# Kernel optimization log

Measured on AMD Instinct MI355X. Metric: run time of the kernel, lower is better.

Reference implementation:

```python
import jax, jax.numpy as jnp
import numpy as np

IN_DIM, H_DIM = 512, 1024
SEQ, BS = 512, 128

def setup_inputs() -> dict:
    key = jax.random.key(0)
    ks = jax.random.split(key, 8)
    d = IN_DIM + H_DIM
    s = 1.0 / np.sqrt(d)
    return {
        "x": jax.random.normal(ks[0], (SEQ, BS, IN_DIM), jnp.float32),
        "h0": jax.random.normal(ks[1], (BS, H_DIM), jnp.float32),
        # Linear weights stored as [in_features, out_features] for x @ W
        "Wz": jax.random.uniform(ks[2], (d, H_DIM), jnp.float32, -s, s),
        "bz": jax.random.uniform(ks[3], (H_DIM,), jnp.float32, -s, s),
        "Wr": jax.random.uniform(ks[4], (d, H_DIM), jnp.float32, -s, s),
        "br": jax.random.uniform(ks[5], (H_DIM,), jnp.float32, -s, s),
        "Wh": jax.random.uniform(ks[6], (d, H_DIM), jnp.float32, -s, s),
        "bh": jax.random.uniform(ks[7], (H_DIM,), jnp.float32, -s, s),
    }

def reference(x, h0, Wz, bz, Wr, br, Wh, bh):
    # Non-standard GRU cell: softmax-activated update/reset gates.
    def step(h, xt):
        hx = jnp.concatenate([h, xt], axis=1)          # [bs, h+in]
        z = jax.nn.softmax(hx @ Wz + bz, axis=1)       # [bs, h]
        r = jax.nn.softmax(hx @ Wr + br, axis=1)
        rhx = jnp.concatenate([r * h, xt], axis=1)
        h_new = (1.0 - z) * h + z * jnp.tanh(rhx @ Wh + bh)
        return h_new, h_new
    _, out = jax.lax.scan(step, h0, x)                 # out: [seq, bs, h]
    return out
```

## Files before the change

### kernel.cpp

```cpp
#include <hip/hip_runtime.h>
#include <hip/hip_bf16.h>


#define SEQ 512
#define BS 128
#define IN_DIM 512
#define H_DIM 1024
#define DTOT 1536
#define NZR 2048

typedef __attribute__((ext_vector_type(8))) short bfrag;
typedef __attribute__((ext_vector_type(4))) float facc;

__device__ __forceinline__ unsigned short f2bf(float f) {
    unsigned int u = __float_as_uint(f);
    unsigned int r = (u + 0x7FFFu + ((u >> 16) & 1u)) >> 16;
    return (unsigned short)r;
}


__global__ void cvt_w(const float* __restrict__ Wz, const float* __restrict__ Wr,
                      const float* __restrict__ Wh,
                      unsigned short* __restrict__ wzr, unsigned short* __restrict__ wh) {
    size_t i = (size_t)blockIdx.x * 256 + threadIdx.x;
    if (i >= (size_t)3072 * DTOT) return;
    int k = (int)(i % DTOT);
    int n = (int)(i / DTOT);
    float v;
    if (n < 1024)       v = Wz[(size_t)k * H_DIM + n];
    else if (n < 2048)  v = Wr[(size_t)k * H_DIM + (n - 1024)];
    else                v = Wh[(size_t)k * H_DIM + (n - 2048)];
    unsigned short b = f2bf(v);
    if (n < 2048) wzr[(size_t)n * DTOT + k] = b;
    else          wh[(size_t)(n - 2048) * DTOT + k] = b;
}

__global__ void cvt_x(const float4* __restrict__ x, unsigned long long* __restrict__ xb) {
    size_t i = (size_t)blockIdx.x * 256 + threadIdx.x;
    if (i >= (size_t)SEQ * BS * IN_DIM / 4) return;
    float4 v = x[i];
    unsigned long long p = (unsigned long long)f2bf(v.x)
                         | ((unsigned long long)f2bf(v.y) << 16)
                         | ((unsigned long long)f2bf(v.z) << 32)
                         | ((unsigned long long)f2bf(v.w) << 48);
    xb[i] = p;
}

__global__ void init_h(const float* __restrict__ h0, float* __restrict__ hf,
                       unsigned short* __restrict__ hb) {
    int i = blockIdx.x * 256 + threadIdx.x;
    if (i >= BS * H_DIM) return;
    float v = h0[i];
    hf[i] = v;
    hb[i] = f2bf(v);
}


__global__ __launch_bounds__(256) void gemm_zr(
    const unsigned short* __restrict__ hb,
    const unsigned short* __restrict__ xb,
    const unsigned short* __restrict__ wt,
    const float* __restrict__ bz, const float* __restrict__ br,
    float* __restrict__ pre) {
    const int lane = threadIdx.x & 63;
    const int wid  = threadIdx.x >> 6;
    const int nBase = blockIdx.x * 64 + wid * 16;
    const int mBase = blockIdx.y * 64;
    const int lm = lane & 15;
    const int kq = lane >> 4;
    facc acc[4];
    #pragma unroll
    for (int i = 0; i < 4; ++i) acc[i] = (facc){0.f, 0.f, 0.f, 0.f};
    const unsigned short* wrow = wt + (size_t)(nBase + lm) * DTOT + kq * 8;
    #pragma unroll 4
    for (int kc = 0; kc < DTOT; kc += 32) {
        const unsigned short* asrc;
        int astride;
        if (kc < 1024) { asrc = hb + kc;          astride = H_DIM; }
        else           { asrc = xb + (kc - 1024); astride = IN_DIM; }
        bfrag b = *(const bfrag*)(wrow + kc);
        #pragma unroll
        for (int mt = 0; mt < 4; ++mt) {
            bfrag a = *(const bfrag*)(asrc + (size_t)(mBase + mt * 16 + lm) * astride + kq * 8);
            acc[mt] = __builtin_amdgcn_mfma_f32_16x16x32_bf16(a, b, acc[mt], 0, 0, 0);
        }
    }
    const int col = nBase + lm;
    const float bias = (col < 1024) ? bz[col] : br[col - 1024];
    #pragma unroll
    for (int mt = 0; mt < 4; ++mt) {
        #pragma unroll
        for (int r = 0; r < 4; ++r) {
            int row = mBase + mt * 16 + kq * 4 + r;
            pre[(size_t)row * NZR + col] = acc[mt][r] + bias;
        }
    }
}

__global__ __launch_bounds__(256) void softmax_rh(
    const float* __restrict__ pre, const float* __restrict__ hf,
    float* __restrict__ z, unsigned short* __restrict__ rh) {
    const int b = blockIdx.x;
    const int tid = threadIdx.x;
    const int lane = tid & 63, wid = tid >> 6;
    const float* prow = pre + (size_t)b * NZR;
    float zl[4], rl[4];
    float mz = -1e30f, mr = -1e30f;
    #pragma unroll
    for (int j = 0; j < 4; ++j) {
        int n = tid + j * 256;
        zl[j] = prow[n];
        rl[j] = prow[1024 + n];
        mz = fmaxf(mz, zl[j]); mr = fmaxf(mr, rl[j]);
    }
    #pragma unroll
    for (int off = 32; off; off >>= 1) {
        mz = fmaxf(mz, __shfl_down(mz, off, 64));
        mr = fmaxf(mr, __shfl_down(mr, off, 64));
    }
    __shared__ float sm[8];
    if (lane == 0) { sm[wid] = mz; sm[4 + wid] = mr; }
    __syncthreads();
    mz = fmaxf(fmaxf(sm[0], sm[1]), fmaxf(sm[2], sm[3]));
    mr = fmaxf(fmaxf(sm[4], sm[5]), fmaxf(sm[6], sm[7]));
    float sz = 0.f, sr = 0.f;
    #pragma unroll
    for (int j = 0; j < 4; ++j) {
        zl[j] = expf(zl[j] - mz); rl[j] = expf(rl[j] - mr);
        sz += zl[j]; sr += rl[j];
    }
    #pragma unroll
    for (int off = 32; off; off >>= 1) {
        sz += __shfl_down(sz, off, 64);
        sr += __shfl_down(sr, off, 64);
    }
    __shared__ float ss[8];
    if (lane == 0) { ss[wid] = sz; ss[4 + wid] = sr; }
    __syncthreads();
    sz = ss[0] + ss[1] + ss[2] + ss[3];
    sr = ss[4] + ss[5] + ss[6] + ss[7];
    const float inz = 1.0f / sz, inr = 1.0f / sr;
    #pragma unroll
    for (int j = 0; j < 4; ++j) {
        int n = tid + j * 256;
        size_t idx = (size_t)b * H_DIM + n;
        z[idx] = zl[j] * inz;
        rh[idx] = f2bf(rl[j] * inr * hf[idx]);
    }
}

__global__ __launch_bounds__(256) void gemm_h(
    const unsigned short* __restrict__ rh,
    const unsigned short* __restrict__ xb,
    const unsigned short* __restrict__ wt,
    const float* __restrict__ bh,
    const float* __restrict__ z,
    float* __restrict__ hf, unsigned short* __restrict__ hb,
    float* __restrict__ out) {
    const int lane = threadIdx.x & 63;
    const int wid  = threadIdx.x >> 6;
    const int nBase = blockIdx.x * 64 + wid * 16;
    const int mBase = blockIdx.y * 64;
    const int lm = lane & 15;
    const int kq = lane >> 4;
    facc acc[4];
    #pragma unroll
    for (int i = 0; i < 4; ++i) acc[i] = (facc){0.f, 0.f, 0.f, 0.f};
    const unsigned short* wrow = wt + (size_t)(nBase + lm) * DTOT + kq * 8;
    #pragma unroll 4
    for (int kc = 0; kc < DTOT; kc += 32) {
        const unsigned short* asrc;
        int astride;
        if (kc < 1024) { asrc = rh + kc;          astride = H_DIM; }
        else           { asrc = xb + (kc - 1024); astride = IN_DIM; }
        bfrag b = *(const bfrag*)(wrow + kc);
        #pragma unroll
        for (int mt = 0; mt < 4; ++mt) {
            bfrag a = *(const bfrag*)(asrc + (size_t)(mBase + mt * 16 + lm) * astride + kq * 8);
            acc[mt] = __builtin_amdgcn_mfma_f32_16x16x32_bf16(a, b, acc[mt], 0, 0, 0);
        }
    }
    const int col = nBase + lm;
    const float bias = bh[col];
    #pragma unroll
    for (int mt = 0; mt < 4; ++mt) {
        #pragma unroll
        for (int r = 0; r < 4; ++r) {
            int row = mBase + mt * 16 + kq * 4 + r;
            size_t idx = (size_t)row * H_DIM + col;
            float th = tanhf(acc[mt][r] + bias);
            float zv = z[idx];
            float hv = hf[idx];
            float hn = fmaf(zv, th - hv, hv);
            hf[idx] = hn;
            hb[idx] = f2bf(hn);
            out[idx] = hn;
        }
    }
}


extern "C" void kernel_launch(void* const* d_in, const int* in_sizes, int n_in,
                              void* d_out, int out_size, void* d_ws, size_t ws_size,
                              hipStream_t stream) {
    const float* x  = (const float*)d_in[0];
    const float* h0 = (const float*)d_in[1];
    const float* Wz = (const float*)d_in[2];
    const float* bz = (const float*)d_in[3];
    const float* Wr = (const float*)d_in[4];
    const float* br = (const float*)d_in[5];
    const float* Wh = (const float*)d_in[6];
    const float* bh = (const float*)d_in[7];
    float* out = (float*)d_out;

    char* base = (char*)d_ws;
    unsigned short* wzr_t  = (unsigned short*)(base);
    unsigned short* wh_t   = (unsigned short*)(base + 6291456);
    unsigned short* x_bf16 = (unsigned short*)(base + 9437184);
    float*          h_f32  = (float*)         (base + 76546048);
    unsigned short* h_bf16 = (unsigned short*)(base + 77070336);
    unsigned short* rh_b   = (unsigned short*)(base + 77332480);
    float*          pre_zr = (float*)         (base + 77594624);
    float*          z_f32  = (float*)         (base + 78643200);

    cvt_w<<<(3072 * DTOT + 255) / 256, 256, 0, stream>>>(Wz, Wr, Wh, wzr_t, wh_t);
    cvt_x<<<((SEQ * BS * IN_DIM / 4) + 255) / 256, 256, 0, stream>>>(
        (const float4*)x, (unsigned long long*)x_bf16);
    init_h<<<(BS * H_DIM + 255) / 256, 256, 0, stream>>>(h0, h_f32, h_bf16);

    for (int t = 0; t < SEQ; ++t) {
        const unsigned short* xb_t = x_bf16 + (size_t)t * BS * IN_DIM;
        float* out_t = out + (size_t)t * BS * H_DIM;
        gemm_zr<<<dim3(NZR / 64, BS / 64), 256, 0, stream>>>(
            h_bf16, xb_t, wzr_t, bz, br, pre_zr);
        softmax_rh<<<BS, 256, 0, stream>>>(pre_zr, h_f32, z_f32, rh_b);
        gemm_h<<<dim3(H_DIM / 64, BS / 64), 256, 0, stream>>>(
            rh_b, xb_t, wh_t, bh, z_f32, h_f32, h_bf16, out_t);
    }
}
```

Baseline: 34.89 ms.

## Replace per-step kernel launches with persistent cooperative GRU kernel using grid barriers

Replaces the three-kernels-per-timestep loop with one cooperative persistent kernel of 192 blocks. Each block keeps its 16-column weight slice resident in LDS and synchronises timesteps with a software grid barrier. Softmax is computed without max subtraction, using partial row sums reduced across blocks, and the x-projection for the next step is overlapped with the h-gate work. This removes about 1500 launches and the weight reloads from global memory, at the risk of exp overflow without a max and of barrier latency dominating each step.

```diff
diff --git a/kernel.cpp b/kernel.cpp
--- a/kernel.cpp
+++ b/kernel.cpp
@@ -1,5 +1,4 @@
 #include <hip/hip_runtime.h>
-#include <hip/hip_bf16.h>
 
 
 #define SEQ 512
@@ -7,7 +6,9 @@
 #define IN_DIM 512
 #define H_DIM 1024
 #define DTOT 1536
-#define NZR 2048
+#define NB 192
+#define NT 512
+#define WPAD 1544
 
 typedef __attribute__((ext_vector_type(8))) short bfrag;
 typedef __attribute__((ext_vector_type(4))) float facc;
@@ -47,8 +48,9 @@
 }
 
 __global__ void init_h(const float* __restrict__ h0, float* __restrict__ hf,
-                       unsigned short* __restrict__ hb) {
+                       unsigned short* __restrict__ hb, unsigned* __restrict__ bar) {
     int i = blockIdx.x * 256 + threadIdx.x;
+    if (i < 2) bar[i] = 0u;
     if (i >= BS * H_DIM) return;
     float v = h0[i];
     hf[i] = v;
@@ -56,146 +58,214 @@
 }
 
 
-__global__ __launch_bounds__(256) void gemm_zr(
-    const unsigned short* __restrict__ hb,
-    const unsigned short* __restrict__ xb,
-    const unsigned short* __restrict__ wt,
-    const float* __restrict__ bz, const float* __restrict__ br,
-    float* __restrict__ pre) {
-    const int lane = threadIdx.x & 63;
-    const int wid  = threadIdx.x >> 6;
-    const int nBase = blockIdx.x * 64 + wid * 16;
-    const int mBase = blockIdx.y * 64;
-    const int lm = lane & 15;
-    const int kq = lane >> 4;
-    facc acc[4];
-    #pragma unroll
-    for (int i = 0; i < 4; ++i) acc[i] = (facc){0.f, 0.f, 0.f, 0.f};
-    const unsigned short* wrow = wt + (size_t)(nBase + lm) * DTOT + kq * 8;
-    #pragma unroll 4
-    for (int kc = 0; kc < DTOT; kc += 32) {
-        const unsigned short* asrc;
-        int astride;
-        if (kc < 1024) { asrc = hb + kc;          astride = H_DIM; }
-        else           { asrc = xb + (kc - 1024); astride = IN_DIM; }
-        bfrag b = *(const bfrag*)(wrow + kc);
+struct PArgs {
+    const unsigned short* wzr;
+    const unsigned short* wh;
+    const unsigned short* xb;
+    const float* bz;
+    const float* br;
+    const float* bh;
+    float* hf;
+    unsigned short* hb;
+    unsigned short* ub;
+    float* ez;
+    float* szp;
+    float* srp;
+    float* out;
+    unsigned* bar;
+};
+
+__device__ __forceinline__ void gridbar(unsigned* cnt, unsigned* gen) {
+    __builtin_amdgcn_fence(__ATOMIC_RELEASE, "agent");
+    __syncthreads();
+    if (threadIdx.x == 0) {
+        unsigned g = __hip_atomic_load(gen, __ATOMIC_RELAXED, __HIP_MEMORY_SCOPE_AGENT);
+        unsigned a = __hip_atomic_fetch_add(cnt, 1u, __ATOMIC_ACQ_REL, __HIP_MEMORY_SCOPE_AGENT);
+        if (a == (unsigned)(NB - 1)) {
+            __hip_atomic_store(cnt, 0u, __ATOMIC_RELAXED, __HIP_MEMORY_SCOPE_AGENT);
+            __hip_atomic_store(gen, g + 1u, __ATOMIC_RELEASE, __HIP_MEMORY_SCOPE_AGENT);
+        } else {
+            while (__hip_atomic_load(gen, __ATOMIC_RELAXED, __HIP_MEMORY_SCOPE_AGENT) == g) {
+                __builtin_amdgcn_s_sleep(2);
+            }
+        }
+    }
+    __syncthreads();
+    __builtin_amdgcn_fence(__ATOMIC_ACQUIRE, "agent");
+}
+
+__global__ __launch_bounds__(NT, 1) void gru_persistent(PArgs p) {
+    __shared__ unsigned short wlds[16][WPAD];
+    __shared__ float redz[4][BS];
+    __shared__ float redr[4][BS];
+    __shared__ float invz[BS];
+    __shared__ float invr[BS];
+
+    const int tid  = threadIdx.x;
+    const int lane = tid & 63;
+    const int wv   = tid >> 6;
+    const int lm   = lane & 15;
+    const int kq   = lane >> 4;
+    const int blk  = blockIdx.x;
+    const bool is_h = (blk >= 128);
+    const bool is_z = (blk < 64);
+    const int arow = wv * 16 + lm;
+
+    const unsigned short* wsrc = is_h ? (p.wh + (size_t)(blk - 128) * 16 * DTOT)
+                                      : (p.wzr + (size_t)blk * 16 * DTOT);
+    for (int c = tid; c < 16 * 192; c += NT) {
+        int n = c / 192;
+        int o = (c % 192) * 8;
+        *(float4*)&wlds[n][o] = *(const float4*)(wsrc + (size_t)n * DTOT + o);
+    }
+    float bias_l;
+    if (is_h) {
+        bias_l = p.bh[(blk - 128) * 16 + lm];
+    } else {
+        int n = blk * 16 + lm;
+        bias_l = (n < H_DIM) ? p.bz[n] : p.br[n - H_DIM];
+    }
+    __syncthreads();
+
+    unsigned* cnt = p.bar;
+    unsigned* gen = p.bar + 1;
+
+    facc accx = (facc){0.f, 0.f, 0.f, 0.f};
+    if (!is_h) {
+        const unsigned short* ax = p.xb + (size_t)arow * IN_DIM + kq * 8;
         #pragma unroll
-        for (int mt = 0; mt < 4; ++mt) {
-            bfrag a = *(const bfrag*)(asrc + (size_t)(mBase + mt * 16 + lm) * astride + kq * 8);
-            acc[mt] = __builtin_amdgcn_mfma_f32_16x16x32_bf16(a, b, acc[mt], 0, 0, 0);
+        for (int kc = 0; kc < IN_DIM; kc += 32) {
+            bfrag a = *(const bfrag*)(ax + kc);
+            bfrag b = *(const bfrag*)&wlds[lm][H_DIM + kc + kq * 8];
+            accx = __builtin_amdgcn_mfma_f32_16x16x32_bf16(a, b, accx, 0, 0, 0);
         }
     }
-    const int col = nBase + lm;
-    const float bias = (col < 1024) ? bz[col] : br[col - 1024];
-    #pragma unroll
-    for (int mt = 0; mt < 4; ++mt) {
-        #pragma unroll
-        for (int r = 0; r < 4; ++r) {
-            int row = mBase + mt * 16 + kq * 4 + r;
-            pre[(size_t)row * NZR + col] = acc[mt][r] + bias;
+
+    for (int t = 0; t < SEQ; ++t) {
+        const unsigned short* xb_t = p.xb + (size_t)t * BS * IN_DIM;
+
+        if (!is_h) {
+            facc accA = accx;
+            facc accB = (facc){0.f, 0.f, 0.f, 0.f};
+            const unsigned short* ah = p.hb + (size_t)arow * H_DIM + kq * 8;
+            #pragma unroll 4
+            for (int kc = 0; kc < H_DIM; kc += 64) {
+                bfrag a0 = *(const bfrag*)(ah + kc);
+                bfrag b0 = *(const bfrag*)&wlds[lm][kc + kq * 8];
+                accA = __builtin_amdgcn_mfma_f32_16x16x32_bf16(a0, b0, accA, 0, 0, 0);
+                bfrag a1 = *(const bfrag*)(ah + kc + 32);
+                bfrag b1 = *(const bfrag*)&wlds[lm][kc + 32 + kq * 8];
+                accB = __builtin_amdgcn_mfma_f32_16x16x32_bf16(a1, b1, accB, 0, 0, 0);
+            }
+            accA = accA + accB;
+            float e[4], sf[4];
+            #pragma unroll
+            for (int r = 0; r < 4; ++r) {
+                e[r] = expf(accA[r] + bias_l);
+                float s = e[r];
+                s += __shfl_xor(s, 1, 64);
+                s += __shfl_xor(s, 2, 64);
+                s += __shfl_xor(s, 4, 64);
+                s += __shfl_xor(s, 8, 64);
+                sf[r] = s;
+            }
+            if (is_z) {
+                const int col = blk * 16 + lm;
+                #pragma unroll
+                for (int r = 0; r < 4; ++r) {
+                    const int rr = wv * 16 + kq * 4 + r;
+                    p.ez[(size_t)rr * H_DIM + col] = e[r];
+                }
+                if (lm == 0) {
+                    #pragma unroll
+                    for (int r = 0; r < 4; ++r)
+                        p.szp[(size_t)blk * BS + wv * 16 + kq * 4 + r] = sf[r];
+                }
+            } else {
+                const int col = (blk - 64) * 16 + lm;
+                #pragma unroll
+                for (int r = 0; r < 4; ++r) {
+                    const int rr = wv * 16 + kq * 4 + r;
+                    float u = e[r] * p.hf[(size_t)rr * H_DIM + col];
+                    p.ub[(size_t)rr * H_DIM + col] = f2bf(u);
+                }
+                if (lm == 0) {
+                    #pragma unroll
+                    for (int r = 0; r < 4; ++r)
+                        p.srp[(size_t)(blk - 64) * BS + wv * 16 + kq * 4 + r] = sf[r];
+                }
+            }
+        } else {
+            accx = (facc){0.f, 0.f, 0.f, 0.f};
+            const unsigned short* ax = xb_t + (size_t)arow * IN_DIM + kq * 8;
+            #pragma unroll
+            for (int kc = 0; kc < IN_DIM; kc += 32) {
+                bfrag a = *(const bfrag*)(ax + kc);
+                bfrag b = *(const bfrag*)&wlds[lm][H_DIM + kc + kq * 8];
+                accx = __builtin_amdgcn_mfma_f32_16x16x32_bf16(a, b, accx, 0, 0, 0);
+            }
         }
-    }
-}
-
-__global__ __launch_bounds__(256) void softmax_rh(
-    const float* __restrict__ pre, const float* __restrict__ hf,
-    float* __restrict__ z, unsigned short* __restrict__ rh) {
-    const int b = blockIdx.x;
-    const int tid = threadIdx.x;
-    const int lane = tid & 63, wid = tid >> 6;
-    const float* prow = pre + (size_t)b * NZR;
-    float zl[4], rl[4];
-    float mz = -1e30f, mr = -1e30f;
-    #pragma unroll
-    for (int j = 0; j < 4; ++j) {
-        int n = tid + j * 256;
-        zl[j] = prow[n];
-        rl[j] = prow[1024 + n];
-        mz = fmaxf(mz, zl[j]); mr = fmaxf(mr, rl[j]);
-    }
-    #pragma unroll
-    for (int off = 32; off; off >>= 1) {
-        mz = fmaxf(mz, __shfl_down(mz, off, 64));
-        mr = fmaxf(mr, __shfl_down(mr, off, 64));
-    }
-    __shared__ float sm[8];
-    if (lane == 0) { sm[wid] = mz; sm[4 + wid] = mr; }
-    __syncthreads();
-    mz = fmaxf(fmaxf(sm[0], sm[1]), fmaxf(sm[2], sm[3]));
-    mr = fmaxf(fmaxf(sm[4], sm[5]), fmaxf(sm[6], sm[7]));
-    float sz = 0.f, sr = 0.f;
-    #pragma unroll
-    for (int j = 0; j < 4; ++j) {
-        zl[j] = expf(zl[j] - mz); rl[j] = expf(rl[j] - mr);
-        sz += zl[j]; sr += rl[j];
-    }
-    #pragma unroll
-    for (int off = 32; off; off >>= 1) {
-        sz += __shfl_down(sz, off, 64);
-        sr += __shfl_down(sr, off, 64);
-    }
-    __shared__ float ss[8];
-    if (lane == 0) { ss[wid] = sz; ss[4 + wid] = sr; }
-    __syncthreads();
-    sz = ss[0] + ss[1] + ss[2] + ss[3];
-    sr = ss[4] + ss[5] + ss[6] + ss[7];
-    const float inz = 1.0f / sz, inr = 1.0f / sr;
-    #pragma unroll
-    for (int j = 0; j < 4; ++j) {
-        int n = tid + j * 256;
-        size_t idx = (size_t)b * H_DIM + n;
-        z[idx] = zl[j] * inz;
-        rh[idx] = f2bf(rl[j] * inr * hf[idx]);
-    }
-}
-
-__global__ __launch_bounds__(256) void gemm_h(
-    const unsigned short* __restrict__ rh,
-    const unsigned short* __restrict__ xb,
-    const unsigned short* __restrict__ wt,
-    const float* __restrict__ bh,
-    const float* __restrict__ z,
-    float* __restrict__ hf, unsigned short* __restrict__ hb,
-    float* __restrict__ out) {
-    const int lane = threadIdx.x & 63;
-    const int wid  = threadIdx.x >> 6;
-    const int nBase = blockIdx.x * 64 + wid * 16;
-    const int mBase = blockIdx.y * 64;
-    const int lm = lane & 15;
-    const int kq = lane >> 4;
-    facc acc[4];
-    #pragma unroll
-    for (int i = 0; i < 4; ++i) acc[i] = (facc){0.f, 0.f, 0.f, 0.f};
-    const unsigned short* wrow = wt + (size_t)(nBase + lm) * DTOT + kq * 8;
-    #pragma unroll 4
-    for (int kc = 0; kc < DTOT; kc += 32) {
-        const unsigned short* asrc;
-        int astride;
-        if (kc < 1024) { asrc = rh + kc;          astride = H_DIM; }
-        else           { asrc = xb + (kc - 1024); astride = IN_DIM; }
-        bfrag b = *(const bfrag*)(wrow + kc);
-        #pragma unroll
-        for (int mt = 0; mt < 4; ++mt) {
-            bfrag a = *(const bfrag*)(asrc + (size_t)(mBase + mt * 16 + lm) * astride + kq * 8);
-            acc[mt] = __builtin_amdgcn_mfma_f32_16x16x32_bf16(a, b, acc[mt], 0, 0, 0);
+        gridbar(cnt, gen);
+
+        if (is_h) {
+            {
+                const int b = tid & 127;
+                const int g = tid >> 7;
+                float az = 0.f, ar = 0.f;
+                #pragma unroll
+                for (int j = 0; j < 16; ++j) {
+                    az += p.szp[(size_t)(g * 16 + j) * BS + b];
+                    ar += p.srp[(size_t)(g * 16 + j) * BS + b];
+                }
+                redz[g][b] = az;
+                redr[g][b] = ar;
+            }
+            __syncthreads();
+            if (tid < BS) {
+                invz[tid] = 1.f / (redz[0][tid] + redz[1][tid] + redz[2][tid] + redz[3][tid]);
+                invr[tid] = 1.f / (redr[0][tid] + redr[1][tid] + redr[2][tid] + redr[3][tid]);
+            }
+            __syncthreads();
+            facc accA = (facc){0.f, 0.f, 0.f, 0.f};
+            facc accB = (facc){0.f, 0.f, 0.f, 0.f};
+            const unsigned short* au = p.ub + (size_t)arow * H_DIM + kq * 8;
+            #pragma unroll 4
+            for (int kc = 0; kc < H_DIM; kc += 64) {
+                bfrag a0 = *(const bfrag*)(au + kc);
+                bfrag b0 = *(const bfrag*)&wlds[lm][kc + kq * 8];
+                accA = __builtin_amdgcn_mfma_f32_16x16x32_bf16(a0, b0, accA, 0, 0, 0);
+                bfrag a1 = *(const bfrag*)(au + kc + 32);
+                bfrag b1 = *(const bfrag*)&wlds[lm][kc + 32 + kq * 8];
+                accB = __builtin_amdgcn_mfma_f32_16x16x32_bf16(a1, b1, accB, 0, 0, 0);
+            }
+            accA = accA + accB;
+            const int col = (blk - 128) * 16 + lm;
+            float* out_t = p.out + (size_t)t * BS * H_DIM;
+            #pragma unroll
+            for (int r = 0; r < 4; ++r) {
+                const int rr = wv * 16 + kq * 4 + r;
+                const size_t idx = (size_t)rr * H_DIM + col;
+                float pre = accA[r] * invr[rr] + accx[r] + bias_l;
+                float th = tanhf(pre);
+                float zv = p.ez[idx] * invz[rr];
+                float hv = p.hf[idx];
+                float hn = fmaf(zv, th - hv, hv);
+                p.hf[idx] = hn;
+                p.hb[idx] = f2bf(hn);
+                out_t[idx] = hn;
+            }
+        } else if (t + 1 < SEQ) {
+            accx = (facc){0.f, 0.f, 0.f, 0.f};
+            const unsigned short* ax = p.xb + (size_t)(t + 1) * BS * IN_DIM
+                                       + (size_t)arow * IN_DIM + kq * 8;
+            #pragma unroll
+            for (int kc = 0; kc < IN_DIM; kc += 32) {
+                bfrag a = *(const bfrag*)(ax + kc);
+                bfrag b = *(const bfrag*)&wlds[lm][H_DIM + kc + kq * 8];
+                accx = __builtin_amdgcn_mfma_f32_16x16x32_bf16(a, b, accx, 0, 0, 0);
+            }
         }
-    }
-    const int col = nBase + lm;
-    const float bias = bh[col];
-    #pragma unroll
-    for (int mt = 0; mt < 4; ++mt) {
-        #pragma unroll
-        for (int r = 0; r < 4; ++r) {
-            int row = mBase + mt * 16 + kq * 4 + r;
-            size_t idx = (size_t)row * H_DIM + col;
-            float th = tanhf(acc[mt][r] + bias);
-            float zv = z[idx];
-            float hv = hf[idx];
-            float hn = fmaf(zv, th - hv, hv);
-            hf[idx] = hn;
-            hb[idx] = f2bf(hn);
-            out[idx] = hn;
-        }
+        gridbar(cnt, gen);
     }
 }
 
@@ -214,27 +284,28 @@
     float* out = (float*)d_out;
 
     char* base = (char*)d_ws;
-    unsigned short* wzr_t  = (unsigned short*)(base);
-    unsigned short* wh_t   = (unsigned short*)(base + 6291456);
-    unsigned short* x_bf16 = (unsigned short*)(base + 9437184);
-    float*          h_f32  = (float*)         (base + 76546048);
-    unsigned short* h_bf16 = (unsigned short*)(base + 77070336);
-    unsigned short* rh_b   = (unsigned short*)(base + 77332480);
-    float*          pre_zr = (float*)         (base + 77594624);
-    float*          z_f32  = (float*)         (base + 78643200);
+    unsigned short* wzr_t = (unsigned short*)(base);
+    unsigned short* wh_t  = (unsigned short*)(base + 6291456);
+    unsigned short* x_b   = (unsigned short*)(base + 9437184);
+    float*          h_f32 = (float*)         (base + 76546048);
+    unsigned short* h_b   = (unsigned short*)(base + 77070336);
+    unsigned short* u_b   = (unsigned short*)(base + 77332480);
+    float*          ez    = (float*)         (base + 77594624);
+    float*          szp   = (float*)         (base + 78118912);
+    float*          srp   = (float*)         (base + 78151680);
+    unsigned*       bar   = (unsigned*)      (base + 78184448);
 
     cvt_w<<<(3072 * DTOT + 255) / 256, 256, 0, stream>>>(Wz, Wr, Wh, wzr_t, wh_t);
     cvt_x<<<((SEQ * BS * IN_DIM / 4) + 255) / 256, 256, 0, stream>>>(
-        (const float4*)x, (unsigned long long*)x_bf16);
-    init_h<<<(BS * H_DIM + 255) / 256, 256, 0, stream>>>(h0, h_f32, h_bf16);
-
-    for (int t = 0; t < SEQ; ++t) {
-        const unsigned short* xb_t = x_bf16 + (size_t)t * BS * IN_DIM;
-        float* out_t = out + (size_t)t * BS * H_DIM;
-        gemm_zr<<<dim3(NZR / 64, BS / 64), 256, 0, stream>>>(
-            h_bf16, xb_t, wzr_t, bz, br, pre_zr);
-        softmax_rh<<<BS, 256, 0, stream>>>(pre_zr, h_f32, z_f32, rh_b);
-        gemm_h<<<dim3(H_DIM / 64, BS / 64), 256, 0, stream>>>(
-            rh_b, xb_t, wh_t, bh, z_f32, h_f32, h_bf16, out_t);
-    }
-}
+        (const float4*)x, (unsigned long long*)x_b);
+    init_h<<<(BS * H_DIM + 255) / 256, 256, 0, stream>>>(h0, h_f32, h_b, bar);
+
+    PArgs pa;
+    pa.wzr = wzr_t; pa.wh = wh_t; pa.xb = x_b;
+    pa.bz = bz; pa.br = br; pa.bh = bh;
+    pa.hf = h_f32; pa.hb = h_b; pa.ub = u_b; pa.ez = ez;
+    pa.szp = szp; pa.srp = srp; pa.out = out; pa.bar = bar;
+    void* kp[] = { &pa };
+    hipLaunchCooperativeKernel(reinterpret_cast<void*>(gru_persistent),
+                               dim3(NB), dim3(NT), kp, 0, stream);
+}
```

Result: slower. 64.99 ms (+86.3%).
